# Performance work log

Hardware: AMD Instinct MI355X
Metric: run time of the kernel (lower is better)

Reference implementation:

```python
import jax, jax.numpy as jnp
import numpy as np

N_SEG, N_REG, N_EDGE, HID, CHEB_K = 40000, 1000, 640000, 256, 5


def setup_inputs() -> dict:
    key = jax.random.key(0)
    ks = jax.random.split(key, 6)
    return {
        "projected_region_features": jax.random.normal(ks[0], (N_REG, HID), jnp.float32),
        "segment2region_assignment": jax.random.uniform(ks[1], (N_SEG, N_REG), jnp.float32),
        "edge_index": jax.random.randint(ks[2], (2, N_EDGE), 0, N_SEG, dtype=jnp.int64),
        # ChebConv params: one [HID,HID] weight per Chebyshev order + shared bias
        "cheb_W": jax.random.normal(ks[3], (CHEB_K, HID, HID), jnp.float32) / np.sqrt(HID).astype(np.float32),
        "cheb_b": jnp.zeros((HID,), jnp.float32),
        "ln_gamma": jnp.ones((HID,), jnp.float32),
        "ln_beta": jnp.zeros((HID,), jnp.float32),
    }


def _cheb_conv(x, edge_index, W, b):
    """PyG ChebConv with normalization='sym', lambda_max=2.0.
    Scaled Laplacian L_hat = 2L/lam - I = -D^{-1/2} A D^{-1/2} (diag = 0)."""
    N = x.shape[0]
    src, dst = edge_index[0], edge_index[1]
    w = (src != dst).astype(x.dtype)  # remove_self_loops
    deg = jax.ops.segment_sum(w, src, num_segments=N)
    dinv = jnp.where(deg > 0, jax.lax.rsqrt(jnp.where(deg > 0, deg, 1.0)), 0.0)
    norm = -w * dinv[src] * dinv[dst]  # per-edge weight of L_hat

    def prop(t):  # y_i = sum_{(j->i)} norm_e * t_j
        return jax.ops.segment_sum(norm[:, None] * t[src], dst, num_segments=N)

    Tx0 = x
    out = Tx0 @ W[0]
    Tx1 = prop(Tx0)
    out = out + Tx1 @ W[1]
    for k in range(2, W.shape[0]):
        Tx2 = 2.0 * prop(Tx1) - Tx0
        out = out + Tx2 @ W[k]
        Tx0, Tx1 = Tx1, Tx2
    return out + b


def _layer_norm(x, g, b, eps=1e-5):
    mu = jnp.mean(x, axis=-1, keepdims=True)
    var = jnp.mean(jnp.square(x - mu), axis=-1, keepdims=True)
    return (x - mu) * jax.lax.rsqrt(var + eps) * g + b


def reference(projected_region_features, segment2region_assignment, edge_index,
              cheb_W, cheb_b, ln_gamma, ln_beta):
    # [n_seg, n_reg] @ [n_reg, hid] -> [n_seg, hid]
    seg_low_raw = segment2region_assignment @ projected_region_features
    seg_low = _cheb_conv(seg_low_raw, edge_index, cheb_W, cheb_b)
    seg_low = _layer_norm(jax.nn.gelu(seg_low, approximate=False), ln_gamma, ln_beta)
    return (seg_low, seg_low_raw)
```

## Files before the change

kernel.cpp:

```cpp
#include <hip/hip_runtime.h>

#define NSEG 40000
#define NREG 1000
#define NEDGE 640000
#define HID 256
#define KCAT 1280
#define KP1 1024
#define NBLK 157

typedef float f32x4 __attribute__((ext_vector_type(4)));
typedef short s16x8 __attribute__((ext_vector_type(8)));
typedef unsigned short u16x4 __attribute__((ext_vector_type(4)));
typedef unsigned short u16x8 __attribute__((ext_vector_type(8)));

typedef __attribute__((address_space(3))) unsigned int lds_u32;
typedef __attribute__((address_space(1))) const unsigned int glb_u32;

__device__ __forceinline__ void dma16(const void* g, void* l) {
    __builtin_amdgcn_global_load_lds((glb_u32*)g, (lds_u32*)l, 16, 0, 0);
}

__device__ __forceinline__ unsigned short f2bf(float f) {
    unsigned u = __builtin_bit_cast(unsigned, f);
    u += 0x7FFFu + ((u >> 16) & 1u);
    return (unsigned short)(u >> 16);
}
__device__ __forceinline__ float bf2f(unsigned short h) {
    unsigned u = ((unsigned)h) << 16;
    return __builtin_bit_cast(float, u);
}

__device__ __forceinline__ f32x4 mfma16(s16x8 a, s16x8 b, f32x4 c) {
    return __builtin_amdgcn_mfma_f32_16x16x32_bf16(a, b, c, 0, 0, 0);
}

__global__ void detect_kernel(const unsigned int* __restrict__ E, int* flag) {
    int lane = threadIdx.x;
    unsigned v = E[2 * lane + 1];
    unsigned long long m = __ballot(v == 0u);
    if (lane == 0) *flag = (__popcll(m) >= 48) ? 1 : 0;
}

__device__ __forceinline__ int edge_at(const void* E, int idx, int is64) {
    return is64 ? (int)((const long long*)E)[idx] : ((const int*)E)[idx];
}

__global__ __launch_bounds__(256) void deg_cnt_kernel(const void* __restrict__ E,
                                                      const int* __restrict__ flag,
                                                      int* deg, int* cnt) {
    int e = blockIdx.x * 256 + threadIdx.x;
    if (e >= NEDGE) return;
    int is64 = *flag;
    int s = edge_at(E, e, is64);
    int d = edge_at(E, e + NEDGE, is64);
    if (s != d) {
        atomicAdd(&deg[s], 1);
        atomicAdd(&cnt[d], 1);
    }
}

__global__ __launch_bounds__(256) void dinv_kernel(const int* __restrict__ deg,
                                                   float* __restrict__ dinv) {
    int i = blockIdx.x * 256 + threadIdx.x;
    if (i < NSEG) {
        int d = deg[i];
        dinv[i] = d > 0 ? rsqrtf((float)d) : 0.f;
    }
}

__global__ __launch_bounds__(256) void scan1_kernel(const int* __restrict__ cnt,
                                                    int* __restrict__ bsum) {
    __shared__ int sh[256];
    int t = threadIdx.x;
    int i = blockIdx.x * 256 + t;
    sh[t] = (i < NSEG) ? cnt[i] : 0;
    __syncthreads();
    for (int o = 128; o > 0; o >>= 1) {
        if (t < o) sh[t] += sh[t + o];
        __syncthreads();
    }
    if (t == 0) bsum[blockIdx.x] = sh[0];
}

__global__ __launch_bounds__(256) void scan2_kernel(const int* __restrict__ bsum,
                                                    int* __restrict__ boff,
                                                    int* __restrict__ rowptr) {
    __shared__ int sh[256];
    int t = threadIdx.x;
    int v = (t < NBLK) ? bsum[t] : 0;
    sh[t] = v;
    __syncthreads();
    for (int o = 1; o < 256; o <<= 1) {
        int x = 0;
        if (t >= o) x = sh[t - o];
        __syncthreads();
        if (t >= o) sh[t] += x;
        __syncthreads();
    }
    if (t < NBLK) boff[t] = sh[t] - v;
    if (t == 255) rowptr[NSEG] = sh[255];
}

__global__ __launch_bounds__(256) void scan3_kernel(const int* __restrict__ cnt,
                                                    const int* __restrict__ boff,
                                                    int* __restrict__ rowptr,
                                                    int* __restrict__ cursor) {
    __shared__ int sh[256];
    int t = threadIdx.x;
    int i = blockIdx.x * 256 + t;
    int v = (i < NSEG) ? cnt[i] : 0;
    sh[t] = v;
    __syncthreads();
    for (int o = 1; o < 256; o <<= 1) {
        int x = 0;
        if (t >= o) x = sh[t - o];
        __syncthreads();
        if (t >= o) sh[t] += x;
        __syncthreads();
    }
    if (i < NSEG) {
        int p = boff[blockIdx.x] + sh[t] - v;
        rowptr[i] = p;
        cursor[i] = p;
    }
}

__global__ __launch_bounds__(256) void scatter_kernel(const void* __restrict__ E,
                                                      const int* __restrict__ flag,
                                                      const float* __restrict__ dinv,
                                                      int* cursor,
                                                      int* __restrict__ colidx,
                                                      float* __restrict__ val) {
    int e = blockIdx.x * 256 + threadIdx.x;
    if (e >= NEDGE) return;
    int is64 = *flag;
    int s = edge_at(E, e, is64);
    int d = edge_at(E, e + NEDGE, is64);
    if (s != d) {
        int pos = atomicAdd(&cursor[d], 1);
        colidx[pos] = s;
        val[pos] = -dinv[s] * dinv[d];
    }
}

__global__ void prep_pt_kernel(const float* __restrict__ P, unsigned short* __restrict__ Pt) {
    int n = blockIdx.x;
    for (int k = threadIdx.x; k < KP1; k += blockDim.x)
        Pt[(size_t)n * KP1 + k] = (k < NREG) ? f2bf(P[(size_t)k * HID + n]) : (unsigned short)0;
}
__global__ void prep_wt_kernel(const float* __restrict__ W, unsigned short* __restrict__ Wt) {
    int n = blockIdx.x;
    for (int k = threadIdx.x; k < KCAT; k += blockDim.x)
        Wt[(size_t)n * KCAT + k] = f2bf(W[(size_t)k * HID + n]);
}

__global__ __launch_bounds__(512) void gemm1_kernel(const float* __restrict__ S,
                                                    const unsigned short* __restrict__ Pt,
                                                    float* __restrict__ raw,
                                                    unsigned short* __restrict__ xcat) {
    __shared__ unsigned short Af[2][64][40];
    __shared__ unsigned short Bs[2][256 * 32];
    const int tid = threadIdx.x;
    const int lane = tid & 63, wid = tid >> 6;
    const int wm = wid >> 2, wn = wid & 3;
    const int r = lane & 15, q = lane >> 4;
    const int qx = q ^ (r & 3);
    const int m0 = blockIdx.x * 64;
    const int arow = tid >> 3, acol = (tid & 7) * 4;
    const int j0 = 2 * wid, j1 = j0 + 1;
    const int brow0 = j0 * 16 + (lane >> 2), brow1 = j1 * 16 + (lane >> 2);
    const int bcol = (((lane & 3) ^ ((lane >> 2) & 3)) << 3);

    f32x4 acc[2][4] = {};
    const float* aptr = S + (size_t)(m0 + arow) * NREG;

    auto stageB = [&](int c, int kb) {
        dma16(Pt + (size_t)brow0 * KP1 + kb + bcol, &Bs[c][j0 * 512]);
        dma16(Pt + (size_t)brow1 * KP1 + kb + bcol, &Bs[c][j1 * 512]);
    };
    auto loadA = [&](int kb) -> f32x4 {
        int k0 = kb + acol;
        if (k0 + 4 > NREG) k0 = 0;
        return *(const f32x4*)(aptr + k0);
    };
    auto writeA = [&](int c, f32x4 a) {
        u16x4 o = {f2bf(a[0]), f2bf(a[1]), f2bf(a[2]), f2bf(a[3])};
        *(u16x4*)&Af[c][arow][acol] = o;
    };

    stageB(0, 0);
    writeA(0, loadA(0));
    __syncthreads();

    for (int t = 0; t < 32; ++t) {
        const int c = t & 1;
        f32x4 an;
        if (t < 31) {
            stageB(c ^ 1, (t + 1) * 32);
            an = loadA((t + 1) * 32);
        }
        s16x8 af[2], bf[4];
#pragma unroll
        for (int am = 0; am < 2; ++am)
            af[am] = *(const s16x8*)&Af[c][wm * 32 + am * 16 + r][q * 8];
#pragma unroll
        for (int bn = 0; bn < 4; ++bn)
            bf[bn] = *(const s16x8*)&Bs[c][(wn * 64 + bn * 16 + r) * 32 + qx * 8];
#pragma unroll
        for (int am = 0; am < 2; ++am)
#pragma unroll
            for (int bn = 0; bn < 4; ++bn)
                acc[am][bn] = mfma16(af[am], bf[bn], acc[am][bn]);
        if (t < 31) writeA(c ^ 1, an);
        __syncthreads();
    }

#pragma unroll
    for (int am = 0; am < 2; ++am) {
        int rowb = m0 + wm * 32 + am * 16 + q * 4;
#pragma unroll
        for (int bn = 0; bn < 4; ++bn) {
            int col = wn * 64 + bn * 16 + r;
#pragma unroll
            for (int i = 0; i < 4; ++i) {
                float v = acc[am][bn][i];
                raw[(size_t)(rowb + i) * HID + col] = v;
                xcat[(size_t)(rowb + i) * KCAT + col] = f2bf(v);
            }
        }
    }
}

__global__ __launch_bounds__(256) void prop_kernel(unsigned short* xcat,
                                                   const int* __restrict__ rowptr,
                                                   const int* __restrict__ colidx,
                                                   const float* __restrict__ val,
                                                   int inOff, int outOff, int subOff,
                                                   float scale) {
    int g = blockIdx.x * 4 + (threadIdx.x >> 6);
    int lane = threadIdx.x & 63;
    int e0 = rowptr[g], e1 = rowptr[g + 1];
    float a0 = 0.f, a1 = 0.f, a2 = 0.f, a3 = 0.f;
    const unsigned short* xin = xcat + inOff + lane * 4;
    for (int base = e0; base < e1; base += 64) {
        int m = e1 - base;
        if (m > 64) m = 64;
        int cc = 0;
        float vv = 0.f;
        if (lane < m) {
            cc = colidx[base + lane];
            vv = val[base + lane];
        }
        int i = 0;
        for (; i + 8 <= m; i += 8) {
            u16x4 t[8];
#pragma unroll
            for (int j = 0; j < 8; ++j) {
                int c = __shfl(cc, i + j);
                t[j] = *(const u16x4*)(xin + (size_t)c * KCAT);
            }
#pragma unroll
            for (int j = 0; j < 8; ++j) {
                float v = __shfl(vv, i + j);
                a0 += v * bf2f(t[j][0]);
                a1 += v * bf2f(t[j][1]);
                a2 += v * bf2f(t[j][2]);
                a3 += v * bf2f(t[j][3]);
            }
        }
        for (; i < m; ++i) {
            int c = __shfl(cc, i);
            float v = __shfl(vv, i);
            u16x4 t = *(const u16x4*)(xin + (size_t)c * KCAT);
            a0 += v * bf2f(t[0]);
            a1 += v * bf2f(t[1]);
            a2 += v * bf2f(t[2]);
            a3 += v * bf2f(t[3]);
        }
    }
    a0 *= scale; a1 *= scale; a2 *= scale; a3 *= scale;
    if (subOff >= 0) {
        u16x4 p = *(const u16x4*)(xcat + (size_t)g * KCAT + subOff + lane * 4);
        a0 -= bf2f(p[0]); a1 -= bf2f(p[1]); a2 -= bf2f(p[2]); a3 -= bf2f(p[3]);
    }
    u16x4 o = {f2bf(a0), f2bf(a1), f2bf(a2), f2bf(a3)};
    *(u16x4*)(xcat + (size_t)g * KCAT + outOff + lane * 4) = o;
}

__global__ __launch_bounds__(512) void gemm2_kernel(const unsigned short* __restrict__ xcat,
                                                    const unsigned short* __restrict__ Wt,
                                                    const float* __restrict__ bias,
                                                    const float* __restrict__ gamma,
                                                    const float* __restrict__ beta,
                                                    float* __restrict__ outp) {
    __shared__ unsigned short Af[2][64 * 32];
    __shared__ unsigned short Bs[2][256 * 32];
    __shared__ float rs[64][4];
    __shared__ float rss[64][4];
    const int tid = threadIdx.x;
    const int lane = tid & 63, wid = tid >> 6;
    const int wm = wid >> 2, wn = wid & 3;
    const int r = lane & 15, q = lane >> 4;
    const int qx = q ^ (r & 3);
    const int m0 = blockIdx.x * 64;
    const int j0 = 2 * wid, j1 = j0 + 1;
    const int brow0 = j0 * 16 + (lane >> 2), brow1 = j1 * 16 + (lane >> 2);
    const int arowd = wid * 16 + (lane >> 2);
    const int bcol = (((lane & 3) ^ ((lane >> 2) & 3)) << 3);

    f32x4 acc[2][4] = {};

    auto stage = [&](int c, int kb) {
        dma16(Wt + (size_t)brow0 * KCAT + kb + bcol, &Bs[c][j0 * 512]);
        dma16(Wt + (size_t)brow1 * KCAT + kb + bcol, &Bs[c][j1 * 512]);
        if (wid < 4)
            dma16(xcat + (size_t)(m0 + arowd) * KCAT + kb + bcol, &Af[c][wid * 512]);
    };

    stage(0, 0);
    __syncthreads();

    for (int t = 0; t < 40; ++t) {
        const int c = t & 1;
        if (t < 39) stage(c ^ 1, (t + 1) * 32);
        s16x8 af[2], bf[4];
#pragma unroll
        for (int am = 0; am < 2; ++am)
            af[am] = *(const s16x8*)&Af[c][(wm * 32 + am * 16 + r) * 32 + qx * 8];
#pragma unroll
        for (int bn = 0; bn < 4; ++bn)
            bf[bn] = *(const s16x8*)&Bs[c][(wn * 64 + bn * 16 + r) * 32 + qx * 8];
#pragma unroll
        for (int am = 0; am < 2; ++am)
#pragma unroll
            for (int bn = 0; bn < 4; ++bn)
                acc[am][bn] = mfma16(af[am], bf[bn], acc[am][bn]);
        __syncthreads();
    }

    float bc[4], gm[4], bt[4];
#pragma unroll
    for (int bn = 0; bn < 4; ++bn) {
        int col = wn * 64 + bn * 16 + r;
        bc[bn] = bias[col];
        gm[bn] = gamma[col];
        bt[bn] = beta[col];
    }
#pragma unroll
    for (int am = 0; am < 2; ++am) {
#pragma unroll
        for (int i = 0; i < 4; ++i) {
            float s = 0.f, ss = 0.f;
#pragma unroll
            for (int bn = 0; bn < 4; ++bn) {
                float v = acc[am][bn][i] + bc[bn];
                v = 0.5f * v * (1.f + erff(v * 0.70710678118654752f));
                acc[am][bn][i] = v;
                s += v;
                ss += v * v;
            }
#pragma unroll
            for (int msk = 1; msk < 16; msk <<= 1) {
                s += __shfl_xor(s, msk);
                ss += __shfl_xor(ss, msk);
            }
            if (r == 0) {
                int row = wm * 32 + am * 16 + q * 4 + i;
                rs[row][wn] = s;
                rss[row][wn] = ss;
            }
        }
    }
    __syncthreads();
#pragma unroll
    for (int am = 0; am < 2; ++am) {
#pragma unroll
        for (int i = 0; i < 4; ++i) {
            int row = wm * 32 + am * 16 + q * 4 + i;
            float s = rs[row][0] + rs[row][1] + rs[row][2] + rs[row][3];
            float ss = rss[row][0] + rss[row][1] + rss[row][2] + rss[row][3];
            float mu = s * (1.f / HID);
            float var = ss * (1.f / HID) - mu * mu;
            float inv = rsqrtf(var + 1e-5f);
#pragma unroll
            for (int bn = 0; bn < 4; ++bn) {
                int col = wn * 64 + bn * 16 + r;
                outp[(size_t)(m0 + row) * HID + col] = (acc[am][bn][i] - mu) * inv * gm[bn] + bt[bn];
            }
        }
    }
}

extern "C" void kernel_launch(void* const* d_in, const int* in_sizes, int n_in,
                              void* d_out, int out_size, void* d_ws, size_t ws_size,
                              hipStream_t stream) {
    const float* P     = (const float*)d_in[0];
    const float* S     = (const float*)d_in[1];
    const void*  E     = d_in[2];
    const float* W     = (const float*)d_in[3];
    const float* bias  = (const float*)d_in[4];
    const float* gamma = (const float*)d_in[5];
    const float* beta  = (const float*)d_in[6];

    float* out = (float*)d_out;
    float* raw = out + (size_t)NSEG * HID;

    char* ws = (char*)d_ws;
    size_t off = 0;
    auto alloc = [&](size_t bytes) -> void* {
        void* p = ws + off;
        off += (bytes + 255) & ~(size_t)255;
        return p;
    };
    unsigned short* xcat   = (unsigned short*)alloc((size_t)NSEG * KCAT * 2);
    unsigned short* Pt     = (unsigned short*)alloc((size_t)HID * KP1 * 2);
    unsigned short* Wt     = (unsigned short*)alloc((size_t)HID * KCAT * 2);
    int*            deg    = (int*)alloc((size_t)NSEG * 4);
    float*          dinv   = (float*)alloc((size_t)NSEG * 4);
    int*            cnt    = (int*)alloc((size_t)NSEG * 4);
    int*            rowptr = (int*)alloc((size_t)(NSEG + 1) * 4);
    int*            cursor = (int*)alloc((size_t)NSEG * 4);
    int*            colidx = (int*)alloc((size_t)NEDGE * 4);
    float*          val    = (float*)alloc((size_t)NEDGE * 4);
    int*            bsum   = (int*)alloc((size_t)NBLK * 4);
    int*            boff   = (int*)alloc((size_t)NBLK * 4);
    int*            flag   = (int*)alloc(256);
    if (off > ws_size) return;

    hipMemsetAsync(deg, 0, (size_t)NSEG * 4, stream);
    hipMemsetAsync(cnt, 0, (size_t)NSEG * 4, stream);

    detect_kernel<<<1, 64, 0, stream>>>((const unsigned int*)E, flag);
    prep_pt_kernel<<<HID, 256, 0, stream>>>(P, Pt);
    prep_wt_kernel<<<HID, 256, 0, stream>>>(W, Wt);

    deg_cnt_kernel<<<NEDGE / 256, 256, 0, stream>>>(E, flag, deg, cnt);
    dinv_kernel<<<(NSEG + 255) / 256, 256, 0, stream>>>(deg, dinv);
    scan1_kernel<<<NBLK, 256, 0, stream>>>(cnt, bsum);
    scan2_kernel<<<1, 256, 0, stream>>>(bsum, boff, rowptr);
    scan3_kernel<<<NBLK, 256, 0, stream>>>(cnt, boff, rowptr, cursor);
    scatter_kernel<<<NEDGE / 256, 256, 0, stream>>>(E, flag, dinv, cursor, colidx, val);

    gemm1_kernel<<<NSEG / 64, 512, 0, stream>>>(S, Pt, raw, xcat);

    prop_kernel<<<NSEG / 4, 256, 0, stream>>>(xcat, rowptr, colidx, val, 0 * HID, 1 * HID, -1, 1.f);
    prop_kernel<<<NSEG / 4, 256, 0, stream>>>(xcat, rowptr, colidx, val, 1 * HID, 2 * HID, 0 * HID, 2.f);
    prop_kernel<<<NSEG / 4, 256, 0, stream>>>(xcat, rowptr, colidx, val, 2 * HID, 3 * HID, 1 * HID, 2.f);
    prop_kernel<<<NSEG / 4, 256, 0, stream>>>(xcat, rowptr, colidx, val, 3 * HID, 4 * HID, 2 * HID, 2.f);

    gemm2_kernel<<<NSEG / 64, 512, 0, stream>>>(xcat, Wt, bias, gamma, beta, out);
}
```

Measured before the change: 445.1 us.

## Load GEMM operands directly from global into registers, dropping LDS staging

New measurement: 623.4 us. 40.0% more time.

```diff
diff --git a/kernel.cpp b/kernel.cpp
--- a/kernel.cpp
+++ b/kernel.cpp
@@ -12,13 +12,6 @@
 typedef short s16x8 __attribute__((ext_vector_type(8)));
 typedef unsigned short u16x4 __attribute__((ext_vector_type(4)));
 typedef unsigned short u16x8 __attribute__((ext_vector_type(8)));
-
-typedef __attribute__((address_space(3))) unsigned int lds_u32;
-typedef __attribute__((address_space(1))) const unsigned int glb_u32;
-
-__device__ __forceinline__ void dma16(const void* g, void* l) {
-    __builtin_amdgcn_global_load_lds((glb_u32*)g, (lds_u32*)l, 16, 0, 0);
-}
 
 __device__ __forceinline__ unsigned short f2bf(float f) {
     unsigned u = __builtin_bit_cast(unsigned, f);
@@ -154,65 +147,66 @@
         Wt[(size_t)n * KCAT + k] = f2bf(W[(size_t)k * HID + n]);
 }
 
+struct AB1 {
+    f32x4 a[2][2];
+    u16x8 b[4];
+};
+
 __global__ __launch_bounds__(512) void gemm1_kernel(const float* __restrict__ S,
                                                     const unsigned short* __restrict__ Pt,
                                                     float* __restrict__ raw,
                                                     unsigned short* __restrict__ xcat) {
-    __shared__ unsigned short Af[2][64][40];
-    __shared__ unsigned short Bs[2][256 * 32];
     const int tid = threadIdx.x;
     const int lane = tid & 63, wid = tid >> 6;
     const int wm = wid >> 2, wn = wid & 3;
     const int r = lane & 15, q = lane >> 4;
-    const int qx = q ^ (r & 3);
     const int m0 = blockIdx.x * 64;
-    const int arow = tid >> 3, acol = (tid & 7) * 4;
-    const int j0 = 2 * wid, j1 = j0 + 1;
-    const int brow0 = j0 * 16 + (lane >> 2), brow1 = j1 * 16 + (lane >> 2);
-    const int bcol = (((lane & 3) ^ ((lane >> 2) & 3)) << 3);
+
+    const float* a0p = S + (size_t)(m0 + wm * 32 + r) * NREG;
+    const float* a1p = S + (size_t)(m0 + wm * 32 + 16 + r) * NREG;
+    const unsigned short* bp[4];
+#pragma unroll
+    for (int bn = 0; bn < 4; ++bn)
+        bp[bn] = Pt + (size_t)(wn * 64 + bn * 16 + r) * KP1;
+
+    auto load_ab = [&](int kb) -> AB1 {
+        AB1 o;
+        int k0 = kb + q * 8;
+        int ka = (k0 + 8 > NREG) ? 0 : k0;
+        o.a[0][0] = *(const f32x4*)(a0p + ka);
+        o.a[0][1] = *(const f32x4*)(a0p + ka + 4);
+        o.a[1][0] = *(const f32x4*)(a1p + ka);
+        o.a[1][1] = *(const f32x4*)(a1p + ka + 4);
+#pragma unroll
+        for (int bn = 0; bn < 4; ++bn)
+            o.b[bn] = *(const u16x8*)(bp[bn] + k0);
+        return o;
+    };
 
     f32x4 acc[2][4] = {};
-    const float* aptr = S + (size_t)(m0 + arow) * NREG;
-
-    auto stageB = [&](int c, int kb) {
-        dma16(Pt + (size_t)brow0 * KP1 + kb + bcol, &Bs[c][j0 * 512]);
-        dma16(Pt + (size_t)brow1 * KP1 + kb + bcol, &Bs[c][j1 * 512]);
-    };
-    auto loadA = [&](int kb) -> f32x4 {
-        int k0 = kb + acol;
-        if (k0 + 4 > NREG) k0 = 0;
-        return *(const f32x4*)(aptr + k0);
-    };
-    auto writeA = [&](int c, f32x4 a) {
-        u16x4 o = {f2bf(a[0]), f2bf(a[1]), f2bf(a[2]), f2bf(a[3])};
-        *(u16x4*)&Af[c][arow][acol] = o;
-    };
-
-    stageB(0, 0);
-    writeA(0, loadA(0));
-    __syncthreads();
+    AB1 cur = load_ab(0);
 
     for (int t = 0; t < 32; ++t) {
-        const int c = t & 1;
-        f32x4 an;
-        if (t < 31) {
-            stageB(c ^ 1, (t + 1) * 32);
-            an = loadA((t + 1) * 32);
-        }
-        s16x8 af[2], bf[4];
+        AB1 nxt;
+        if (t < 31) nxt = load_ab((t + 1) * 32);
+        s16x8 af[2];
+#pragma unroll
+        for (int am = 0; am < 2; ++am) {
+            u16x8 tmp;
+#pragma unroll
+            for (int i = 0; i < 4; ++i) {
+                tmp[i]     = f2bf(cur.a[am][0][i]);
+                tmp[i + 4] = f2bf(cur.a[am][1][i]);
+            }
+            af[am] = __builtin_bit_cast(s16x8, tmp);
+        }
 #pragma unroll
         for (int am = 0; am < 2; ++am)
-            af[am] = *(const s16x8*)&Af[c][wm * 32 + am * 16 + r][q * 8];
-#pragma unroll
-        for (int bn = 0; bn < 4; ++bn)
-            bf[bn] = *(const s16x8*)&Bs[c][(wn * 64 + bn * 16 + r) * 32 + qx * 8];
-#pragma unroll
-        for (int am = 0; am < 2; ++am)
 #pragma unroll
             for (int bn = 0; bn < 4; ++bn)
-                acc[am][bn] = mfma16(af[am], bf[bn], acc[am][bn]);
-        if (t < 31) writeA(c ^ 1, an);
-        __syncthreads();
+                acc[am][bn] = mfma16(af[am], __builtin_bit_cast(s16x8, cur.b[bn]), acc[am][bn]);
+        if (t < 31) cur = nxt;
+        if ((t & 3) == 3) __syncthreads();
     }
 
 #pragma unroll
@@ -287,55 +281,57 @@
     *(u16x4*)(xcat + (size_t)g * KCAT + outOff + lane * 4) = o;
 }
 
+struct AB2 {
+    u16x8 a[2];
+    u16x8 b[4];
+};
+
 __global__ __launch_bounds__(512) void gemm2_kernel(const unsigned short* __restrict__ xcat,
                                                     const unsigned short* __restrict__ Wt,
                                                     const float* __restrict__ bias,
                                                     const float* __restrict__ gamma,
                                                     const float* __restrict__ beta,
                                                     float* __restrict__ outp) {
-    __shared__ unsigned short Af[2][64 * 32];
-    __shared__ unsigned short Bs[2][256 * 32];
     __shared__ float rs[64][4];
     __shared__ float rss[64][4];
     const int tid = threadIdx.x;
     const int lane = tid & 63, wid = tid >> 6;
     const int wm = wid >> 2, wn = wid & 3;
     const int r = lane & 15, q = lane >> 4;
-    const int qx = q ^ (r & 3);
     const int m0 = blockIdx.x * 64;
-    const int j0 = 2 * wid, j1 = j0 + 1;
-    const int brow0 = j0 * 16 + (lane >> 2), brow1 = j1 * 16 + (lane >> 2);
-    const int arowd = wid * 16 + (lane >> 2);
-    const int bcol = (((lane & 3) ^ ((lane >> 2) & 3)) << 3);
+
+    const unsigned short* a0p = xcat + (size_t)(m0 + wm * 32 + r) * KCAT;
+    const unsigned short* a1p = xcat + (size_t)(m0 + wm * 32 + 16 + r) * KCAT;
+    const unsigned short* bp[4];
+#pragma unroll
+    for (int bn = 0; bn < 4; ++bn)
+        bp[bn] = Wt + (size_t)(wn * 64 + bn * 16 + r) * KCAT;
+
+    auto load_ab = [&](int kb) -> AB2 {
+        AB2 o;
+        int k0 = kb + q * 8;
+        o.a[0] = *(const u16x8*)(a0p + k0);
+        o.a[1] = *(const u16x8*)(a1p + k0);
+#pragma unroll
+        for (int bn = 0; bn < 4; ++bn)
+            o.b[bn] = *(const u16x8*)(bp[bn] + k0);
+        return o;
+    };
 
     f32x4 acc[2][4] = {};
-
-    auto stage = [&](int c, int kb) {
-        dma16(Wt + (size_t)brow0 * KCAT + kb + bcol, &Bs[c][j0 * 512]);
-        dma16(Wt + (size_t)brow1 * KCAT + kb + bcol, &Bs[c][j1 * 512]);
-        if (wid < 4)
-            dma16(xcat + (size_t)(m0 + arowd) * KCAT + kb + bcol, &Af[c][wid * 512]);
-    };
-
-    stage(0, 0);
-    __syncthreads();
+    AB2 cur = load_ab(0);
 
     for (int t = 0; t < 40; ++t) {
-        const int c = t & 1;
-        if (t < 39) stage(c ^ 1, (t + 1) * 32);
-        s16x8 af[2], bf[4];
+        AB2 nxt;
+        if (t < 39) nxt = load_ab((t + 1) * 32);
 #pragma unroll
         for (int am = 0; am < 2; ++am)
-            af[am] = *(const s16x8*)&Af[c][(wm * 32 + am * 16 + r) * 32 + qx * 8];
-#pragma unroll
-        for (int bn = 0; bn < 4; ++bn)
-            bf[bn] = *(const s16x8*)&Bs[c][(wn * 64 + bn * 16 + r) * 32 + qx * 8];
-#pragma unroll
-        for (int am = 0; am < 2; ++am)
 #pragma unroll
             for (int bn = 0; bn < 4; ++bn)
-                acc[am][bn] = mfma16(af[am], bf[bn], acc[am][bn]);
-        __syncthreads();
+                acc[am][bn] = mfma16(__builtin_bit_cast(s16x8, cur.a[am]),
+                                     __builtin_bit_cast(s16x8, cur.b[bn]), acc[am][bn]);
+        if (t < 39) cur = nxt;
+        if ((t & 3) == 3) __syncthreads();
     }
 
     float bc[4], gm[4], bt[4];
```

## Shrink GEMM tiles to 32 rows with single-buffered LDS

Applied to the files above, without the earlier changes.

New measurement: 492.0 us. 1.11x slower.

```diff
diff --git a/kernel.cpp b/kernel.cpp
--- a/kernel.cpp
+++ b/kernel.cpp
@@ -154,70 +154,58 @@
         Wt[(size_t)n * KCAT + k] = f2bf(W[(size_t)k * HID + n]);
 }
 
-__global__ __launch_bounds__(512) void gemm1_kernel(const float* __restrict__ S,
+__global__ __launch_bounds__(256) void gemm1_kernel(const float* __restrict__ S,
                                                     const unsigned short* __restrict__ Pt,
                                                     float* __restrict__ raw,
                                                     unsigned short* __restrict__ xcat) {
-    __shared__ unsigned short Af[2][64][40];
-    __shared__ unsigned short Bs[2][256 * 32];
+    __shared__ unsigned short As[32 * 32];
+    __shared__ unsigned short Bs[256 * 32];
     const int tid = threadIdx.x;
-    const int lane = tid & 63, wid = tid >> 6;
-    const int wm = wid >> 2, wn = wid & 3;
+    const int lane = tid & 63, wn = tid >> 6;
     const int r = lane & 15, q = lane >> 4;
-    const int qx = q ^ (r & 3);
-    const int m0 = blockIdx.x * 64;
+    const int qx8 = (q ^ (r & 3)) << 3;
+    const int m0 = blockIdx.x * 32;
     const int arow = tid >> 3, acol = (tid & 7) * 4;
-    const int j0 = 2 * wid, j1 = j0 + 1;
-    const int brow0 = j0 * 16 + (lane >> 2), brow1 = j1 * 16 + (lane >> 2);
-    const int bcol = (((lane & 3) ^ ((lane >> 2) & 3)) << 3);
+    const int agr = ((((acol >> 3) ^ (arow & 3)) << 3) | (acol & 7));
+    const int crow = lane >> 2;
+    const int bcol = (((lane & 3) ^ (crow & 3)) << 3);
+    const float* aptr = S + (size_t)(m0 + arow) * NREG;
 
     f32x4 acc[2][4] = {};
-    const float* aptr = S + (size_t)(m0 + arow) * NREG;
-
-    auto stageB = [&](int c, int kb) {
-        dma16(Pt + (size_t)brow0 * KP1 + kb + bcol, &Bs[c][j0 * 512]);
-        dma16(Pt + (size_t)brow1 * KP1 + kb + bcol, &Bs[c][j1 * 512]);
-    };
-    auto loadA = [&](int kb) -> f32x4 {
-        int k0 = kb + acol;
-        if (k0 + 4 > NREG) k0 = 0;
-        return *(const f32x4*)(aptr + k0);
-    };
-    auto writeA = [&](int c, f32x4 a) {
-        u16x4 o = {f2bf(a[0]), f2bf(a[1]), f2bf(a[2]), f2bf(a[3])};
-        *(u16x4*)&Af[c][arow][acol] = o;
-    };
-
-    stageB(0, 0);
-    writeA(0, loadA(0));
-    __syncthreads();
 
     for (int t = 0; t < 32; ++t) {
-        const int c = t & 1;
-        f32x4 an;
-        if (t < 31) {
-            stageB(c ^ 1, (t + 1) * 32);
-            an = loadA((t + 1) * 32);
-        }
-        s16x8 af[2], bf[4];
+        const int kb = t * 32;
+        __syncthreads();
+#pragma unroll
+        for (int k = 0; k < 4; ++k) {
+            int j = wn * 4 + k;
+            dma16(Pt + (size_t)(j * 16 + crow) * KP1 + kb + bcol, &Bs[j * 512]);
+        }
+        {
+            int k0 = kb + acol;
+            if (k0 + 4 > NREG) k0 = 0;
+            f32x4 v = *(const f32x4*)(aptr + k0);
+            u16x4 o = {f2bf(v[0]), f2bf(v[1]), f2bf(v[2]), f2bf(v[3])};
+            *(u16x4*)&As[arow * 32 + agr] = o;
+        }
+        __syncthreads();
+        s16x8 af[2], bfv[4];
 #pragma unroll
         for (int am = 0; am < 2; ++am)
-            af[am] = *(const s16x8*)&Af[c][wm * 32 + am * 16 + r][q * 8];
+            af[am] = *(const s16x8*)&As[(am * 16 + r) * 32 + qx8];
 #pragma unroll
         for (int bn = 0; bn < 4; ++bn)
-            bf[bn] = *(const s16x8*)&Bs[c][(wn * 64 + bn * 16 + r) * 32 + qx * 8];
+            bfv[bn] = *(const s16x8*)&Bs[(wn * 64 + bn * 16 + r) * 32 + qx8];
 #pragma unroll
         for (int am = 0; am < 2; ++am)
 #pragma unroll
             for (int bn = 0; bn < 4; ++bn)
-                acc[am][bn] = mfma16(af[am], bf[bn], acc[am][bn]);
-        if (t < 31) writeA(c ^ 1, an);
-        __syncthreads();
+                acc[am][bn] = mfma16(af[am], bfv[bn], acc[am][bn]);
     }
 
 #pragma unroll
     for (int am = 0; am < 2; ++am) {
-        int rowb = m0 + wm * 32 + am * 16 + q * 4;
+        int rowb = m0 + am * 16 + q * 4;
 #pragma unroll
         for (int bn = 0; bn < 4; ++bn) {
             int col = wn * 64 + bn * 16 + r;
@@ -287,55 +275,51 @@
     *(u16x4*)(xcat + (size_t)g * KCAT + outOff + lane * 4) = o;
 }
 
-__global__ __launch_bounds__(512) void gemm2_kernel(const unsigned short* __restrict__ xcat,
+__global__ __launch_bounds__(256) void gemm2_kernel(const unsigned short* __restrict__ xcat,
                                                     const unsigned short* __restrict__ Wt,
                                                     const float* __restrict__ bias,
                                                     const float* __restrict__ gamma,
                                                     const float* __restrict__ beta,
                                                     float* __restrict__ outp) {
-    __shared__ unsigned short Af[2][64 * 32];
-    __shared__ unsigned short Bs[2][256 * 32];
-    __shared__ float rs[64][4];
-    __shared__ float rss[64][4];
+    __shared__ unsigned short As[32 * 32];
+    __shared__ unsigned short Bs[256 * 32];
+    __shared__ float rs[32][4];
+    __shared__ float rss[32][4];
     const int tid = threadIdx.x;
-    const int lane = tid & 63, wid = tid >> 6;
-    const int wm = wid >> 2, wn = wid & 3;
+    const int lane = tid & 63, wn = tid >> 6;
     const int r = lane & 15, q = lane >> 4;
-    const int qx = q ^ (r & 3);
-    const int m0 = blockIdx.x * 64;
-    const int j0 = 2 * wid, j1 = j0 + 1;
-    const int brow0 = j0 * 16 + (lane >> 2), brow1 = j1 * 16 + (lane >> 2);
-    const int arowd = wid * 16 + (lane >> 2);
-    const int bcol = (((lane & 3) ^ ((lane >> 2) & 3)) << 3);
+    const int qx8 = (q ^ (r & 3)) << 3;
+    const int m0 = blockIdx.x * 32;
+    const int crow = lane >> 2;
+    const int bcol = (((lane & 3) ^ (crow & 3)) << 3);
 
     f32x4 acc[2][4] = {};
 
-    auto stage = [&](int c, int kb) {
-        dma16(Wt + (size_t)brow0 * KCAT + kb + bcol, &Bs[c][j0 * 512]);
-        dma16(Wt + (size_t)brow1 * KCAT + kb + bcol, &Bs[c][j1 * 512]);
-        if (wid < 4)
-            dma16(xcat + (size_t)(m0 + arowd) * KCAT + kb + bcol, &Af[c][wid * 512]);
-    };
-
-    stage(0, 0);
-    __syncthreads();
-
     for (int t = 0; t < 40; ++t) {
-        const int c = t & 1;
-        if (t < 39) stage(c ^ 1, (t + 1) * 32);
-        s16x8 af[2], bf[4];
+        const int kb = t * 32;
+        __syncthreads();
+#pragma unroll
+        for (int k = 0; k < 4; ++k) {
+            int j = wn * 4 + k;
+            dma16(Wt + (size_t)(j * 16 + crow) * KCAT + kb + bcol, &Bs[j * 512]);
+        }
+        if (wn < 2) {
+            int row = m0 + wn * 16 + crow;
+            dma16(xcat + (size_t)row * KCAT + kb + bcol, &As[wn * 512]);
+        }
+        __syncthreads();
+        s16x8 af[2], bfv[4];
 #pragma unroll
         for (int am = 0; am < 2; ++am)
-            af[am] = *(const s16x8*)&Af[c][(wm * 32 + am * 16 + r) * 32 + qx * 8];
+            af[am] = *(const s16x8*)&As[(am * 16 + r) * 32 + qx8];
 #pragma unroll
         for (int bn = 0; bn < 4; ++bn)
-            bf[bn] = *(const s16x8*)&Bs[c][(wn * 64 + bn * 16 + r) * 32 + qx * 8];
+            bfv[bn] = *(const s16x8*)&Bs[(wn * 64 + bn * 16 + r) * 32 + qx8];
 #pragma unroll
         for (int am = 0; am < 2; ++am)
 #pragma unroll
             for (int bn = 0; bn < 4; ++bn)
-                acc[am][bn] = mfma16(af[am], bf[bn], acc[am][bn]);
-        __syncthreads();
+                acc[am][bn] = mfma16(af[am], bfv[bn], acc[am][bn]);
     }
 
     float bc[4], gm[4], bt[4];
@@ -365,7 +349,7 @@
                 ss += __shfl_xor(ss, msk);
             }
             if (r == 0) {
-                int row = wm * 32 + am * 16 + q * 4 + i;
+                int row = am * 16 + q * 4 + i;
                 rs[row][wn] = s;
                 rss[row][wn] = ss;
             }
@@ -376,7 +360,7 @@
     for (int am = 0; am < 2; ++am) {
 #pragma unroll
         for (int i = 0; i < 4; ++i) {
-            int row = wm * 32 + am * 16 + q * 4 + i;
+            int row = am * 16 + q * 4 + i;
             float s = rs[row][0] + rs[row][1] + rs[row][2] + rs[row][3];
             float ss = rss[row][0] + rss[row][1] + rss[row][2] + rss[row][3];
             float mu = s * (1.f / HID);
@@ -441,12 +425,12 @@
     scan3_kernel<<<NBLK, 256, 0, stream>>>(cnt, boff, rowptr, cursor);
     scatter_kernel<<<NEDGE / 256, 256, 0, stream>>>(E, flag, dinv, cursor, colidx, val);
 
-    gemm1_kernel<<<NSEG / 64, 512, 0, stream>>>(S, Pt, raw, xcat);
+    gemm1_kernel<<<NSEG / 32, 256, 0, stream>>>(S, Pt, raw, xcat);
 
     prop_kernel<<<NSEG / 4, 256, 0, stream>>>(xcat, rowptr, colidx, val, 0 * HID, 1 * HID, -1, 1.f);
     prop_kernel<<<NSEG / 4, 256, 0, stream>>>(xcat, rowptr, colidx, val, 1 * HID, 2 * HID, 0 * HID, 2.f);
     prop_kernel<<<NSEG / 4, 256, 0, stream>>>(xcat, rowptr, colidx, val, 2 * HID, 3 * HID, 1 * HID, 2.f);
     prop_kernel<<<NSEG / 4, 256, 0, stream>>>(xcat, rowptr, colidx, val, 3 * HID, 4 * HID, 2 * HID, 2.f);
 
-    gemm2_kernel<<<NSEG / 64, 512, 0, stream>>>(xcat, Wt, bias, gamma, beta, out);
-}
+    gemm2_kernel<<<NSEG / 32, 256, 0, stream>>>(xcat, Wt, bias, gamma, beta, out);
+}
```
